# Kernel optimization log

Measured on AMD Instinct MI355X. Metric: run time of the kernel, lower is better.

Reference implementation:

```python
import jax, jax.numpy as jnp
import numpy as np


def setup_inputs() -> dict:
    key = jax.random.key(0)
    k1, k2, k3 = jax.random.split(key, 3)
    B, S, D = 2, 2048, 1024
    N_COMPRESS, RANK = 64, 64
    x = jax.random.normal(k1, (B, S, D), dtype=jnp.float32)
    router_w = jax.random.normal(k2, (N_COMPRESS, D), dtype=jnp.float32) * (1.0 / np.sqrt(D))
    # compress neurons (orthogonal-init in torch; gaussian scaled is fine for a numeric baseline)
    neurons = jax.random.normal(k3, (N_COMPRESS, D, RANK), dtype=jnp.float32) * (1.0 / np.sqrt(D))
    return {"x": x, "router_w": router_w, "neurons": neurons}


TOP_K = 2


def reference(x, router_w, neurons):
    # x: [B,S,D], router_w: [N,D], neurons: [N,D,R]
    B, S, D = x.shape
    R = neurons.shape[-1]
    scores = jnp.einsum('bsd,nd->bsn', x, router_w)            # [B,S,N]
    topk_scores, topk_idx = jax.lax.top_k(scores, TOP_K)       # [B,S,K]
    topk_weights = jax.nn.softmax(topk_scores, axis=-1)        # [B,S,K]
    output = jnp.zeros((B, S, R), dtype=x.dtype)
    for i in range(TOP_K):  # small fixed loop, mirrors original slot-wise combine
        idx = topk_idx[:, :, i]                                # [B,S]
        sel = neurons[idx]                                     # [B,S,D,R] gather
        proj = jnp.einsum('bsd,bsdr->bsr', x, sel)             # per-token matvec
        output = output + topk_weights[:, :, i:i + 1] * proj
    return output, topk_idx, topk_weights
```

## Files before the change

### kernel.cpp

```cpp
#include <hip/hip_runtime.h>
#include <hip/hip_bf16.h>


typedef unsigned short u16;
typedef unsigned int u32;
typedef __attribute__((ext_vector_type(8))) short short8;
typedef __attribute__((ext_vector_type(4))) float f32x4;

__device__ __forceinline__ float bf2f(u16 u) {
    u32 v = ((u32)u) << 16; float f; __builtin_memcpy(&f, &v, 4); return f;
}
__device__ __forceinline__ u16 f2bf(float f) {
    u32 u; __builtin_memcpy(&u, &f, 4);
    u32 r = u + 0x7fff + ((u >> 16) & 1);
    return (u16)(r >> 16);
}
__device__ __forceinline__ u32 pack2(float a, float b) {
    return ((u32)f2bf(b) << 16) | (u32)f2bf(a);
}

#define T_TOKENS 4096
#define DDIM 1024
#define NEXP 64
#define RDIM 64
#define LCAP 1024
#define OUT_IDX_OFF 262144
#define OUT_W_OFF 270336

struct LdBF {
    const u16* p;
    __device__ __forceinline__ float4 ld4(size_t i) const {
        ushort4 v = *(const ushort4*)(p + i);
        return make_float4(bf2f(v.x), bf2f(v.y), bf2f(v.z), bf2f(v.w));
    }
    __device__ __forceinline__ float ld1(size_t i) const { return bf2f(p[i]); }
};
struct LdF32 {
    const float* p;
    __device__ __forceinline__ float4 ld4(size_t i) const { return *(const float4*)(p + i); }
    __device__ __forceinline__ float ld1(size_t i) const { return p[i]; }
};

__device__ __forceinline__ int detect_f32(const u16* x, int* lds_cnt) {
    if (threadIdx.x == 0) *lds_cnt = 0;
    __syncthreads();
    if (threadIdx.x < 256) {
        unsigned e = (x[threadIdx.x] >> 7) & 0xFF;
        if (e >= 0x68 && e <= 0x88) atomicAdd(lds_cnt, 1);
    }
    __syncthreads();
    int f = (*lds_cnt < 200) ? 1 : 0;
    __syncthreads();
    return f;
}

template <class LD>
__device__ __forceinline__ void score_body(LD xld, LD rwld,
                                           float* xs , float* wt ,
                                           float* sc , float* Sb) {
    const int tid = threadIdx.x;
    const int g = blockIdx.x >> 1;
    const int kh = blockIdx.x & 1;
    const size_t t0 = (size_t)g * 8;
    const int kbase = kh * 512;
    const int wv = tid >> 6;
    const int lane = tid & 63;
    const int tg = lane & 1;
    const int eg = (lane >> 1) & 7;
    const int kql = (lane >> 4) & 3;
    const int dd = 4 * kql + 16 * wv;
    const int kc0 = blockIdx.x & 7;

    const int sm = tid >> 4;
    const int sd4 = (tid & 15) * 4;

    float acc[4][8];
#pragma unroll
    for (int mi = 0; mi < 4; ++mi)
#pragma unroll
        for (int ei = 0; ei < 8; ++ei) acc[mi][ei] = 0.f;

    float4 px;
    if (tid < 128) px = xld.ld4((t0 + sm) * DDIM + kbase + kc0 * 64 + sd4);
    float4 pw[4];
#pragma unroll
    for (int h = 0; h < 4; ++h) {
        int i4 = tid + h * 256;
        pw[h] = rwld.ld4((size_t)(i4 >> 4) * DDIM + kbase + kc0 * 64 + (i4 & 15) * 4);
    }

    for (int i = 0; i < 8; ++i) {
        if (i > 0) __syncthreads();
        if (tid < 128) *(float4*)&xs[sm * 68 + sd4] = px;
#pragma unroll
        for (int h = 0; h < 4; ++h) {
            int i4 = tid + h * 256;
            *(float4*)&wt[(i4 >> 4) * 68 + (i4 & 15) * 4] = pw[h];
        }
        __syncthreads();

        if (i < 7) {
            int kn = kbase + ((i + 1 + kc0) & 7) * 64;
            if (tid < 128) px = xld.ld4((t0 + sm) * DDIM + kn + sd4);
#pragma unroll
            for (int h = 0; h < 4; ++h) {
                int i4 = tid + h * 256;
                pw[h] = rwld.ld4((size_t)(i4 >> 4) * DDIM + kn + (i4 & 15) * 4);
            }
        }

        float4 xv[4], wv4[8];
#pragma unroll
        for (int mi = 0; mi < 4; ++mi)
            xv[mi] = *(const float4*)&xs[(tg + 2 * mi) * 68 + dd];
#pragma unroll
        for (int ei = 0; ei < 8; ++ei)
            wv4[ei] = *(const float4*)&wt[(eg + 8 * ei) * 68 + dd];
#pragma unroll
        for (int mi = 0; mi < 4; ++mi)
#pragma unroll
            for (int ei = 0; ei < 8; ++ei)
                acc[mi][ei] += xv[mi].x * wv4[ei].x + xv[mi].y * wv4[ei].y +
                               xv[mi].z * wv4[ei].z + xv[mi].w * wv4[ei].w;
    }

#pragma unroll
    for (int mi = 0; mi < 4; ++mi)
#pragma unroll
        for (int ei = 0; ei < 8; ++ei) {
            float v = acc[mi][ei];
            v += __shfl_xor(v, 16, 64);
            v += __shfl_xor(v, 32, 64);
            acc[mi][ei] = v;
        }
    __syncthreads();

    for (int w = 0; w < 4; ++w) {
        if (wv == w && kql == 0) {
#pragma unroll
            for (int mi = 0; mi < 4; ++mi)
#pragma unroll
                for (int ei = 0; ei < 8; ++ei) {
                    int idx = (tg + 2 * mi) * 65 + eg + 8 * ei;
                    sc[idx] = (w == 0) ? acc[mi][ei] : sc[idx] + acc[mi][ei];
                }
        }
        __syncthreads();
    }

    if (tid < 128) {
        int t = tid >> 4, e4 = (tid & 15) * 4;
        const float* s = &sc[t * 65 + e4];
        float4 v = make_float4(s[0], s[1], s[2], s[3]);
        *(float4*)&Sb[((size_t)kh * T_TOKENS + t0 + t) * 64 + e4] = v;
    }
}

__global__ __launch_bounds__(256, 4) void score_part(const void* x, const void* rw,
                                                     float* Sb) {
    __shared__ float xs[8 * 68];
    __shared__ float wt[64 * 68];
    __shared__ float sc[8 * 65];
    __shared__ int dc;
    int f = detect_f32((const u16*)x, &dc);
    if (f)
        score_body(LdF32{(const float*)x}, LdF32{(const float*)rw}, xs, wt, sc, Sb);
    else
        score_body(LdBF{(const u16*)x}, LdBF{(const u16*)rw}, xs, wt, sc, Sb);
}

__global__ __launch_bounds__(256) void topk_softmax(const float* Sb, float* out,
                                                    float* wsW, int* wsCnt,
                                                    int* wsList) {
    int t = blockIdx.x * 256 + threadIdx.x;
    const float* s0 = Sb + (size_t)t * 64;
    const float* s1 = Sb + ((size_t)T_TOKENS + t) * 64;
    float best = -1e30f, secv = -1e30f;
    int bi = 0, si = 0;
    for (int j = 0; j < NEXP; j += 4) {
        float4 a = *(const float4*)(s0 + j);
        float4 b = *(const float4*)(s1 + j);
        float v0 = a.x + b.x, v1 = a.y + b.y, v2 = a.z + b.z, v3 = a.w + b.w;
        if (v0 > best) { secv = best; si = bi; best = v0; bi = j; }
        else if (v0 > secv) { secv = v0; si = j; }
        if (v1 > best) { secv = best; si = bi; best = v1; bi = j + 1; }
        else if (v1 > secv) { secv = v1; si = j + 1; }
        if (v2 > best) { secv = best; si = bi; best = v2; bi = j + 2; }
        else if (v2 > secv) { secv = v2; si = j + 2; }
        if (v3 > best) { secv = best; si = bi; best = v3; bi = j + 3; }
        else if (v3 > secv) { secv = v3; si = j + 3; }
    }
    float w0 = 1.0f / (1.0f + expf(secv - best));
    float w1 = 1.0f - w0;
    out[OUT_IDX_OFF + (size_t)t * 2 + 0] = (float)bi;
    out[OUT_IDX_OFF + (size_t)t * 2 + 1] = (float)si;
    out[OUT_W_OFF + (size_t)t * 2 + 0] = w0;
    out[OUT_W_OFF + (size_t)t * 2 + 1] = w1;
    wsW[t * 2 + 0] = w0;
    wsW[t * 2 + 1] = w1;
    int p0 = atomicAdd(&wsCnt[bi], 1);
    if (p0 < LCAP) wsList[bi * LCAP + p0] = t * 2 + 0;
    int p1 = atomicAdd(&wsCnt[si], 1);
    if (p1 < LCAP) wsList[si * LCAP + p1] = t * 2 + 1;
}

template <class LD>
__device__ __forceinline__ void egemm_body(LD xld, LD nld,
                                           const int* wsCnt, const int* wsList,
                                           float* P,
                                           u16* Ab , u16* Bb ,
                                           int* eL ) {
    const int tid = threadIdx.x;
    const int e = blockIdx.x >> 3;
    const int oct = blockIdx.x & 7;
    const int cntE = min(wsCnt[e], LCAP);
    if (cntE <= 0) return;
    const int wv = tid >> 6;
    const int lane = tid & 63;
    const int l15 = lane & 15, quad = lane >> 4;
    const size_t nbase = (size_t)e * (DDIM * RDIM);
    const int k0 = oct * 128;

    for (int j = tid; j < cntE; j += 256) eL[j] = wsList[e * LCAP + j];

    {
        const int rq = tid & 15;
        const int kpB = tid >> 4;
        u32* bb = (u32*)Bb;
#pragma unroll
        for (int h = 0; h < 4; ++h) {
            int kp = kpB + h * 16;
            float4 g0 = nld.ld4(nbase + (size_t)(k0 + 2 * kp) * RDIM + rq * 4);
            float4 g1 = nld.ld4(nbase + (size_t)(k0 + 2 * kp + 1) * RDIM + rq * 4);
            bb[(rq * 4 + 0) * 68 + kp] = pack2(g0.x, g1.x);
            bb[(rq * 4 + 1) * 68 + kp] = pack2(g0.y, g1.y);
            bb[(rq * 4 + 2) * 68 + kp] = pack2(g0.z, g1.z);
            bb[(rq * 4 + 3) * 68 + kp] = pack2(g0.w, g1.w);
        }
    }
    __syncthreads();

    const int rowA = tid >> 4;
    const int kqA = tid & 15;
    const int ntiles = (cntE + 15) >> 4;

    float4 a0, a1;
    {
        int t2r = eL[min(rowA, cntE - 1)];
        size_t xrow = (size_t)(t2r >> 1) * DDIM + k0;
        a0 = xld.ld4(xrow + kqA * 8);
        a1 = xld.ld4(xrow + kqA * 8 + 4);
    }

    for (int ti = 0; ti < ntiles; ++ti) {
        const int base = ti * 16;
        const int valid = min(16, cntE - base);
        if (ti > 0) __syncthreads();
        {
            uint4 w;
            w.x = pack2(a0.x, a0.y);
            w.y = pack2(a0.z, a0.w);
            w.z = pack2(a1.x, a1.y);
            w.w = pack2(a1.z, a1.w);
            *(uint4*)&((u32*)Ab)[rowA * 68 + kqA * 4] = w;
        }
        __syncthreads();
        if (ti + 1 < ntiles) {
            int t2r = eL[min(base + 16 + rowA, cntE - 1)];
            size_t xrow = (size_t)(t2r >> 1) * DDIM + k0;
            a0 = xld.ld4(xrow + kqA * 8);
            a1 = xld.ld4(xrow + kqA * 8 + 4);
        }

        f32x4 acc = {0.f, 0.f, 0.f, 0.f};
#pragma unroll
        for (int ko = 0; ko < 4; ++ko) {
            int kofs = ko * 32 + quad * 8;
            short8 bfr = *(const short8*)&Bb[(16 * wv + l15) * 136 + kofs];
            short8 af = *(const short8*)&Ab[l15 * 136 + kofs];
            acc = __builtin_amdgcn_mfma_f32_16x16x32_bf16(af, bfr, acc, 0, 0, 0);
        }

#pragma unroll
        for (int reg = 0; reg < 4; ++reg) {
            int m = quad * 4 + reg;
            if (m < valid) {
                int t2 = eL[base + m];
                P[(size_t)t2 * 512 + oct * 64 + 16 * wv + l15] = acc[reg];
            }
        }
    }
}

__global__ __launch_bounds__(256, 2) void expert_gemm(const void* x, const void* neurons,
                                                      const int* wsCnt, const int* wsList,
                                                      float* P) {
    __shared__ u16 Ab[16 * 136];
    __shared__ u16 Bb[64 * 136];
    __shared__ int eL[LCAP];
    __shared__ int dc;
    int f = detect_f32((const u16*)x, &dc);
    if (f)
        egemm_body(LdF32{(const float*)x}, LdF32{(const float*)neurons}, wsCnt, wsList, P, Ab, Bb, eL);
    else
        egemm_body(LdBF{(const u16*)x}, LdBF{(const u16*)neurons}, wsCnt, wsList, P, Ab, Bb, eL);
}

__global__ __launch_bounds__(256) void combine(const float* P, const float* wsW,
                                               float* out) {
    int i = blockIdx.x * 256 + threadIdx.x;
    int t = i >> 6, r = i & 63;
    const float* p0 = P + (size_t)(2 * t) * 512 + r;
    const float* p1 = P + (size_t)(2 * t + 1) * 512 + r;
    float s0 = 0.f, s1 = 0.f;
#pragma unroll
    for (int o = 0; o < 8; ++o) {
        s0 += p0[o * 64];
        s1 += p1[o * 64];
    }
    out[i] = wsW[2 * t] * s0 + wsW[2 * t + 1] * s1;
}

extern "C" void kernel_launch(void* const* d_in, const int* in_sizes, int n_in,
                              void* d_out, int out_size, void* d_ws, size_t ws_size,
                              hipStream_t stream) {
    const void* x = d_in[0];
    const void* rw = d_in[1];
    const void* neurons = d_in[2];
    float* out = (float*)d_out;

    char* wsc = (char*)d_ws;
    float* wsW = (float*)wsc;
    int* wsCnt = (int*)(wsc + 32 * 1024);
    int* wsList = (int*)((char*)wsCnt + 256);
    float* Sb = (float*)(wsc + (1 << 20));
    float* P = (float*)(wsc + (4 << 20));

    hipMemsetAsync(wsCnt, 0, 256, stream);
    score_part<<<1024, 256, 0, stream>>>(x, rw, Sb);
    topk_softmax<<<16, 256, 0, stream>>>(Sb, out, wsW, wsCnt, wsList);
    expert_gemm<<<512, 256, 0, stream>>>(x, neurons, wsCnt, wsList, P);
    combine<<<1024, 256, 0, stream>>>(P, wsW, out);
}
```

Measured before the change: 125.4 us.

## Fuse top-k softmax into score kernel via last-arriver atomic flag

```diff
diff --git a/kernel.cpp b/kernel.cpp
--- a/kernel.cpp
+++ b/kernel.cpp
@@ -57,7 +57,9 @@
 template <class LD>
 __device__ __forceinline__ void score_body(LD xld, LD rwld,
                                            float* xs , float* wt ,
-                                           float* sc , float* Sb) {
+                                           float* sc , int* farr,
+                                           float* Sb, float* out, float* wsW,
+                                           int* wsCnt, int* wsList, int* flags) {
     const int tid = threadIdx.x;
     const int g = blockIdx.x >> 1;
     const int kh = blockIdx.x & 1;
@@ -154,54 +156,66 @@
         float4 v = make_float4(s[0], s[1], s[2], s[3]);
         *(float4*)&Sb[((size_t)kh * T_TOKENS + t0 + t) * 64 + e4] = v;
     }
+
+    __threadfence();
+    __syncthreads();
+    if (tid == 0) *farr = atomicAdd(&flags[g], 1);
+    __syncthreads();
+    if (*farr == 1) {
+        __threadfence();
+        const int t = tid >> 5;
+        const int l = tid & 31;
+        const float* so = Sb + ((size_t)(kh ^ 1) * T_TOKENS + t0 + t) * 64;
+        float v0 = sc[t * 65 + 2 * l] + so[2 * l];
+        float v1 = sc[t * 65 + 2 * l + 1] + so[2 * l + 1];
+        float best, sec;
+        int bi, si;
+        if (v1 > v0) { best = v1; bi = 2 * l + 1; sec = v0; si = 2 * l; }
+        else         { best = v0; bi = 2 * l;     sec = v1; si = 2 * l + 1; }
+#pragma unroll
+        for (int s = 1; s < 32; s <<= 1) {
+            float pb = __shfl_xor(best, s, 64);
+            int pib = __shfl_xor(bi, s, 64);
+            float ps = __shfl_xor(sec, s, 64);
+            int pis = __shfl_xor(si, s, 64);
+            if (pb > best || (pb == best && pib < bi)) { sec = best; si = bi; best = pb; bi = pib; }
+            else if (pb > sec || (pb == sec && pib < si)) { sec = pb; si = pib; }
+            if (ps > best || (ps == best && pis < bi)) { sec = best; si = bi; best = ps; bi = pis; }
+            else if (ps > sec || (ps == sec && pis < si)) { sec = ps; si = pis; }
+        }
+        if (l == 0) {
+            float w0 = 1.0f / (1.0f + expf(sec - best));
+            float w1 = 1.0f - w0;
+            size_t tt = t0 + t;
+            out[OUT_IDX_OFF + tt * 2 + 0] = (float)bi;
+            out[OUT_IDX_OFF + tt * 2 + 1] = (float)si;
+            out[OUT_W_OFF + tt * 2 + 0] = w0;
+            out[OUT_W_OFF + tt * 2 + 1] = w1;
+            wsW[tt * 2 + 0] = w0;
+            wsW[tt * 2 + 1] = w1;
+            int p0 = atomicAdd(&wsCnt[bi], 1);
+            if (p0 < LCAP) wsList[bi * LCAP + p0] = (int)(tt * 2 + 0);
+            int p1 = atomicAdd(&wsCnt[si], 1);
+            if (p1 < LCAP) wsList[si * LCAP + p1] = (int)(tt * 2 + 1);
+        }
+    }
 }
 
 __global__ __launch_bounds__(256, 4) void score_part(const void* x, const void* rw,
-                                                     float* Sb) {
+                                                     float* Sb, float* out, float* wsW,
+                                                     int* wsCnt, int* wsList, int* flags) {
     __shared__ float xs[8 * 68];
     __shared__ float wt[64 * 68];
     __shared__ float sc[8 * 65];
     __shared__ int dc;
+    __shared__ int farr;
     int f = detect_f32((const u16*)x, &dc);
     if (f)
-        score_body(LdF32{(const float*)x}, LdF32{(const float*)rw}, xs, wt, sc, Sb);
+        score_body(LdF32{(const float*)x}, LdF32{(const float*)rw}, xs, wt, sc, &farr,
+                   Sb, out, wsW, wsCnt, wsList, flags);
     else
-        score_body(LdBF{(const u16*)x}, LdBF{(const u16*)rw}, xs, wt, sc, Sb);
-}
-
-__global__ __launch_bounds__(256) void topk_softmax(const float* Sb, float* out,
-                                                    float* wsW, int* wsCnt,
-                                                    int* wsList) {
-    int t = blockIdx.x * 256 + threadIdx.x;
-    const float* s0 = Sb + (size_t)t * 64;
-    const float* s1 = Sb + ((size_t)T_TOKENS + t) * 64;
-    float best = -1e30f, secv = -1e30f;
-    int bi = 0, si = 0;
-    for (int j = 0; j < NEXP; j += 4) {
-        float4 a = *(const float4*)(s0 + j);
-        float4 b = *(const float4*)(s1 + j);
-        float v0 = a.x + b.x, v1 = a.y + b.y, v2 = a.z + b.z, v3 = a.w + b.w;
-        if (v0 > best) { secv = best; si = bi; best = v0; bi = j; }
-        else if (v0 > secv) { secv = v0; si = j; }
-        if (v1 > best) { secv = best; si = bi; best = v1; bi = j + 1; }
-        else if (v1 > secv) { secv = v1; si = j + 1; }
-        if (v2 > best) { secv = best; si = bi; best = v2; bi = j + 2; }
-        else if (v2 > secv) { secv = v2; si = j + 2; }
-        if (v3 > best) { secv = best; si = bi; best = v3; bi = j + 3; }
-        else if (v3 > secv) { secv = v3; si = j + 3; }
-    }
-    float w0 = 1.0f / (1.0f + expf(secv - best));
-    float w1 = 1.0f - w0;
-    out[OUT_IDX_OFF + (size_t)t * 2 + 0] = (float)bi;
-    out[OUT_IDX_OFF + (size_t)t * 2 + 1] = (float)si;
-    out[OUT_W_OFF + (size_t)t * 2 + 0] = w0;
-    out[OUT_W_OFF + (size_t)t * 2 + 1] = w1;
-    wsW[t * 2 + 0] = w0;
-    wsW[t * 2 + 1] = w1;
-    int p0 = atomicAdd(&wsCnt[bi], 1);
-    if (p0 < LCAP) wsList[bi * LCAP + p0] = t * 2 + 0;
-    int p1 = atomicAdd(&wsCnt[si], 1);
-    if (p1 < LCAP) wsList[si * LCAP + p1] = t * 2 + 1;
+        score_body(LdBF{(const u16*)x}, LdBF{(const u16*)rw}, xs, wt, sc, &farr,
+                   Sb, out, wsW, wsCnt, wsList, flags);
 }
 
 template <class LD>
@@ -332,13 +346,13 @@
     char* wsc = (char*)d_ws;
     float* wsW = (float*)wsc;
     int* wsCnt = (int*)(wsc + 32 * 1024);
-    int* wsList = (int*)((char*)wsCnt + 256);
+    int* flags = (int*)(wsc + 32 * 1024 + 256);
+    int* wsList = (int*)(wsc + 32 * 1024 + 2304);
     float* Sb = (float*)(wsc + (1 << 20));
     float* P = (float*)(wsc + (4 << 20));
 
-    hipMemsetAsync(wsCnt, 0, 256, stream);
-    score_part<<<1024, 256, 0, stream>>>(x, rw, Sb);
-    topk_softmax<<<16, 256, 0, stream>>>(Sb, out, wsW, wsCnt, wsList);
+    hipMemsetAsync(wsCnt, 0, 2304, stream);
+    score_part<<<1024, 256, 0, stream>>>(x, rw, Sb, out, wsW, wsCnt, wsList, flags);
     expert_gemm<<<512, 256, 0, stream>>>(x, neurons, wsCnt, wsList, P);
     combine<<<1024, 256, 0, stream>>>(P, wsW, out);
 }
```

After: 251.9 us. 2.01x slower.

## Prefetch x rows two tiles ahead in expert GEMM; spread topk over more blocks

Applied to the files above, without the earlier changes.

```diff
diff --git a/kernel.cpp b/kernel.cpp
--- a/kernel.cpp
+++ b/kernel.cpp
@@ -169,10 +169,10 @@
         score_body(LdBF{(const u16*)x}, LdBF{(const u16*)rw}, xs, wt, sc, Sb);
 }
 
-__global__ __launch_bounds__(256) void topk_softmax(const float* Sb, float* out,
-                                                    float* wsW, int* wsCnt,
-                                                    int* wsList) {
-    int t = blockIdx.x * 256 + threadIdx.x;
+__global__ __launch_bounds__(64) void topk_softmax(const float* Sb, float* out,
+                                                   float* wsW, int* wsCnt,
+                                                   int* wsList) {
+    int t = blockIdx.x * 64 + threadIdx.x;
     const float* s0 = Sb + (size_t)t * 64;
     const float* s1 = Sb + ((size_t)T_TOKENS + t) * 64;
     float best = -1e30f, secv = -1e30f;
@@ -244,12 +244,19 @@
     const int kqA = tid & 15;
     const int ntiles = (cntE + 15) >> 4;
 
-    float4 a0, a1;
+    float4 c0, c1, n0, n1;
     {
         int t2r = eL[min(rowA, cntE - 1)];
         size_t xrow = (size_t)(t2r >> 1) * DDIM + k0;
-        a0 = xld.ld4(xrow + kqA * 8);
-        a1 = xld.ld4(xrow + kqA * 8 + 4);
+        c0 = xld.ld4(xrow + kqA * 8);
+        c1 = xld.ld4(xrow + kqA * 8 + 4);
+    }
+    n0 = c0; n1 = c1;
+    if (ntiles > 1) {
+        int t2r = eL[min(16 + rowA, cntE - 1)];
+        size_t xrow = (size_t)(t2r >> 1) * DDIM + k0;
+        n0 = xld.ld4(xrow + kqA * 8);
+        n1 = xld.ld4(xrow + kqA * 8 + 4);
     }
 
     for (int ti = 0; ti < ntiles; ++ti) {
@@ -258,18 +265,18 @@
         if (ti > 0) __syncthreads();
         {
             uint4 w;
-            w.x = pack2(a0.x, a0.y);
-            w.y = pack2(a0.z, a0.w);
-            w.z = pack2(a1.x, a1.y);
-            w.w = pack2(a1.z, a1.w);
+            w.x = pack2(c0.x, c0.y);
+            w.y = pack2(c0.z, c0.w);
+            w.z = pack2(c1.x, c1.y);
+            w.w = pack2(c1.z, c1.w);
             *(uint4*)&((u32*)Ab)[rowA * 68 + kqA * 4] = w;
         }
         __syncthreads();
-        if (ti + 1 < ntiles) {
-            int t2r = eL[min(base + 16 + rowA, cntE - 1)];
+        if (ti + 2 < ntiles) {
+            int t2r = eL[min(base + 32 + rowA, cntE - 1)];
             size_t xrow = (size_t)(t2r >> 1) * DDIM + k0;
-            a0 = xld.ld4(xrow + kqA * 8);
-            a1 = xld.ld4(xrow + kqA * 8 + 4);
+            c0 = xld.ld4(xrow + kqA * 8);
+            c1 = xld.ld4(xrow + kqA * 8 + 4);
         }
 
         f32x4 acc = {0.f, 0.f, 0.f, 0.f};
@@ -289,6 +296,10 @@
                 P[(size_t)t2 * 512 + oct * 64 + 16 * wv + l15] = acc[reg];
             }
         }
+
+        float4 s0 = c0, s1 = c1;
+        c0 = n0; c1 = n1;
+        n0 = s0; n1 = s1;
     }
 }
 
@@ -332,13 +343,13 @@
     char* wsc = (char*)d_ws;
     float* wsW = (float*)wsc;
     int* wsCnt = (int*)(wsc + 32 * 1024);
-    int* wsList = (int*)((char*)wsCnt + 256);
+    int* wsList = (int*)(wsc + 32 * 1024 + 256);
     float* Sb = (float*)(wsc + (1 << 20));
     float* P = (float*)(wsc + (4 << 20));
 
     hipMemsetAsync(wsCnt, 0, 256, stream);
     score_part<<<1024, 256, 0, stream>>>(x, rw, Sb);
-    topk_softmax<<<16, 256, 0, stream>>>(Sb, out, wsW, wsCnt, wsList);
+    topk_softmax<<<64, 64, 0, stream>>>(Sb, out, wsW, wsCnt, wsList);
     expert_gemm<<<512, 256, 0, stream>>>(x, neurons, wsCnt, wsList, P);
     combine<<<1024, 256, 0, stream>>>(P, wsW, out);
 }
```

Measured after the change: 123.9 us. About the same (-1.2%).
